# Kernel tuning notes

Measured on AMD Instinct MI355X. Metric: run time of the kernel, lower is better.

Reference implementation:

```python
import jax, jax.numpy as jnp
import numpy as np

DIM = 1024
HEADS = 16
HEAD_DIM = DIM // HEADS
SCALE = DIM ** (-0.5)  # note: module scales by full dim, not head_dim


def setup_inputs() -> dict:
    key = jax.random.key(0)
    k1, k2, k3, k4 = jax.random.split(key, 4)
    B, N = 4, 2048
    x = jax.random.normal(k1, (B, N, DIM), dtype=jnp.float32)
    # nn.Linear(dim, 3*dim, bias=False): weight [3*dim, dim]
    w_qkv = jax.random.normal(k2, (3 * DIM, DIM), dtype=jnp.float32) * (DIM ** -0.5)
    # nn.Linear(dim, dim) with bias
    w_out = jax.random.normal(k3, (DIM, DIM), dtype=jnp.float32) * (DIM ** -0.5)
    b_out = jax.random.normal(k4, (DIM,), dtype=jnp.float32) * 0.01
    return {"x": x, "w_qkv": w_qkv, "w_out": w_out, "b_out": b_out}


def reference(x, w_qkv, w_out, b_out):
    b, n, _ = x.shape
    qkv = jnp.einsum('bnd,ed->bne', x, w_qkv)  # [b, n, 3*dim]
    # rearrange 'b n (qkv h d) -> qkv b h n d'
    qkv = qkv.reshape(b, n, 3, HEADS, HEAD_DIM)
    q, k, v = (qkv[:, :, i].transpose(0, 2, 1, 3) for i in range(3))  # [b, h, n, d]
    dots = jnp.einsum('bhid,bhjd->bhij', q, k) * SCALE
    attn = jax.nn.softmax(dots, axis=-1)
    out = jnp.einsum('bhij,bhjd->bhid', attn, v)
    out = out.transpose(0, 2, 1, 3).reshape(b, n, HEADS * HEAD_DIM)  # [b, n, dim]
    return jnp.einsum('bnd,ed->bne', out, w_out) + b_out
```

## Files before the change

### kernel.cpp

```cpp
#include <hip/hip_runtime.h>

typedef __bf16 bf16_t;
typedef __bf16 bf16x2 __attribute__((ext_vector_type(2)));
typedef __bf16 bf16x4 __attribute__((ext_vector_type(4)));
typedef __bf16 bf16x8 __attribute__((ext_vector_type(8)));
typedef float floatx4 __attribute__((ext_vector_type(4)));

__device__ __forceinline__ void gll16(const void* g, void* l) {
  __builtin_amdgcn_global_load_lds(
      (const __attribute__((address_space(1))) void*)g,
      (__attribute__((address_space(3))) void*)l, 16, 0, 0);
}

__device__ __forceinline__ bf16x8 cvt8(const float4 a, const float4 b) {
  bf16x8 v;
  v[0] = (bf16_t)a.x; v[1] = (bf16_t)a.y; v[2] = (bf16_t)a.z; v[3] = (bf16_t)a.w;
  v[4] = (bf16_t)b.x; v[5] = (bf16_t)b.y; v[6] = (bf16_t)b.z; v[7] = (bf16_t)b.w;
  return v;
}

__global__ __launch_bounds__(256)
void cvt_f32_bf16(const float* __restrict__ src, bf16_t* __restrict__ dst, int n8)
{
  const int i = blockIdx.x * 256 + threadIdx.x;
  if (i < n8) {
    const float4 a = ((const float4*)src)[2 * i];
    const float4 b = ((const float4*)src)[2 * i + 1];
    *(bf16x8*)(dst + (size_t)i * 8) = cvt8(a, b);
  }
}

template<bool A32, bool W32, bool C32>
__global__ __launch_bounds__(256, 2)
void gemm_bt(const void* __restrict__ Av, const void* __restrict__ Wv,
             const float* __restrict__ bias, void* __restrict__ Cv,
             int M, int Nf, int K, int lda)
{
  __shared__ __align__(16) bf16_t lA[128 * 32];
  __shared__ __align__(16) bf16_t lB[128 * 32];

  const int tid  = threadIdx.x;
  const int wave = tid >> 6;
  const int lane = tid & 63;
  const int q    = lane >> 4;
  const int ln   = lane & 15;
  const int wm   = wave >> 1, wn = wave & 1;

  const int mtiles = M >> 7;
  const int mt = blockIdx.x % mtiles;
  const int nt = blockIdx.x / mtiles;
  const int m0 = mt << 7, n0 = nt << 7;

  floatx4 acc[4][4] = {};

  for (int k0 = 0; k0 < K; k0 += 32) {
    if constexpr (A32) {
      const float* Af = (const float*)Av;
#pragma unroll
      for (int sub = 0; sub < 2; ++sub) {
        const int r  = sub * 64 + (tid >> 2);
        const int c8 = tid & 3;
        const float* s = Af + (size_t)(m0 + r) * lda + k0 + c8 * 8;
        const float4 f0 = *(const float4*)s;
        const float4 f1 = *(const float4*)(s + 4);
        *(bf16x8*)(lA + r * 32 + (c8 ^ ((r >> 1) & 3)) * 8) = cvt8(f0, f1);
      }
    } else {
      const bf16_t* Ab = (const bf16_t*)Av;
#pragma unroll
      for (int half = 0; half < 2; ++half) {
        const int rbase = half * 64 + wave * 16;
        const int r  = rbase + (lane >> 2);
        const int gc = (lane & 3) ^ ((r >> 1) & 3);
        gll16(Ab + (size_t)(m0 + r) * lda + k0 + gc * 8, lA + rbase * 32);
      }
    }
    if constexpr (W32) {
      const float* Wf = (const float*)Wv;
#pragma unroll
      for (int sub = 0; sub < 2; ++sub) {
        const int r  = sub * 64 + (tid >> 2);
        const int c8 = tid & 3;
        const float* s = Wf + (size_t)(n0 + r) * K + k0 + c8 * 8;
        const float4 f0 = *(const float4*)s;
        const float4 f1 = *(const float4*)(s + 4);
        *(bf16x8*)(lB + r * 32 + (c8 ^ ((r >> 1) & 3)) * 8) = cvt8(f0, f1);
      }
    } else {
      const bf16_t* Wb = (const bf16_t*)Wv;
#pragma unroll
      for (int half = 0; half < 2; ++half) {
        const int rbase = half * 64 + wave * 16;
        const int r  = rbase + (lane >> 2);
        const int gc = (lane & 3) ^ ((r >> 1) & 3);
        gll16(Wb + (size_t)(n0 + r) * K + k0 + gc * 8, lB + rbase * 32);
      }
    }
    __syncthreads();

    bf16x8 af[4], bfr[4];
#pragma unroll
    for (int i = 0; i < 4; ++i) {
      const int r = wm * 64 + i * 16 + ln;
      af[i] = *(const bf16x8*)(lA + r * 32 + (q ^ ((r >> 1) & 3)) * 8);
    }
#pragma unroll
    for (int j = 0; j < 4; ++j) {
      const int r = wn * 64 + j * 16 + ln;
      bfr[j] = *(const bf16x8*)(lB + r * 32 + (q ^ ((r >> 1) & 3)) * 8);
    }
#pragma unroll
    for (int i = 0; i < 4; ++i)
#pragma unroll
      for (int j = 0; j < 4; ++j)
        acc[i][j] = __builtin_amdgcn_mfma_f32_16x16x32_bf16(af[i], bfr[j], acc[i][j], 0, 0, 0);
    __syncthreads();
  }

#pragma unroll
  for (int j = 0; j < 4; ++j) {
    const int col = n0 + wn * 64 + j * 16 + ln;
    const float bv = bias ? bias[col] : 0.0f;
#pragma unroll
    for (int i = 0; i < 4; ++i) {
      const int row = m0 + wm * 64 + i * 16 + q * 4;
#pragma unroll
      for (int r = 0; r < 4; ++r) {
        const float val = acc[i][j][r] + bv;
        if constexpr (C32)
          ((float*)Cv)[(size_t)(row + r) * Nf + col] = val;
        else
          ((bf16_t*)Cv)[(size_t)(row + r) * Nf + col] = (bf16_t)val;
      }
    }
  }
}

__global__ __launch_bounds__(256, 2)
void attn_kernel(bf16_t* __restrict__ qkv)
{
  __shared__ __align__(16) bf16_t lK[128 * 64];
  __shared__ __align__(16) bf16_t lVT[64 * 128];
  __shared__ __align__(16) bf16_t lP[128 * 136];

  const int tid  = threadIdx.x;
  const int wave = tid >> 6;
  const int lane = tid & 63;
  const int q  = lane >> 4;
  const int ln = lane & 15;
  const int wm = wave >> 1, wn = wave & 1;

  const int bx = blockIdx.x;
  const int qt = bx & 15;
  const int h  = (bx >> 4) & 15;
  const int b  = bx >> 8;

  bf16_t* Qbase = qkv + (size_t)(b * 2048 + qt * 128) * 3072 + h * 64;
  const bf16_t* Kbase = qkv + (size_t)(b * 2048) * 3072 + 1024 + h * 64;
  const bf16_t* Vbase = qkv + (size_t)(b * 2048) * 3072 + 2048 + h * 64;

#pragma unroll
  for (int t = 0; t < 4; ++t) {
    const int rbase = t * 32 + wave * 8;
    const int r  = rbase + (lane >> 3);
    const int gc = (lane & 7) ^ (r & 7);
    gll16(Qbase + (size_t)r * 3072 + gc * 8, lP + rbase * 64);
  }
  __syncthreads();

  bf16x8 qf[4][2];
#pragma unroll
  for (int i = 0; i < 4; ++i) {
    const int r = wm * 64 + i * 16 + ln;
#pragma unroll
    for (int kt = 0; kt < 2; ++kt) {
      const int c = (kt * 4 + q) ^ (r & 7);
      qf[i][kt] = *(const bf16x8*)(lP + r * 64 + c * 8);
    }
  }
  __syncthreads();

  floatx4 accO[4][2] = {};
  floatx4 accS[4] = {};

  bf16x8 ones;
#pragma unroll
  for (int j = 0; j < 8; ++j) ones[j] = (bf16_t)1.0f;

  for (int jt = 0; jt < 16; ++jt) {
    const int j0 = jt * 128;

#pragma unroll
    for (int t = 0; t < 4; ++t) {
      const int rbase = t * 32 + wave * 8;
      const int r  = rbase + (lane >> 3);
      const int gc = (lane & 7) ^ (r & 7);
      gll16(Kbase + (size_t)(j0 + r) * 3072 + gc * 8, lK + rbase * 64);
    }

    {
      const int p = lane;
#pragma unroll
      for (int it = 0; it < 2; ++it) {
        const int c = wave + it * 4;
        const bf16_t* src = Vbase + (size_t)(j0 + 2 * p) * 3072 + c * 8;
        const bf16x8 v0 = *(const bf16x8*)(src);
        const bf16x8 v1 = *(const bf16x8*)(src + 3072);
#pragma unroll
        for (int j = 0; j < 8; ++j) {
          const int d  = c * 8 + j;
          const int ch = (p >> 2) ^ (d & 7);
          bf16x2 pr;
          pr[0] = v0[j];
          pr[1] = v1[j];
          *(bf16x2*)(lVT + d * 128 + ch * 8 + ((2 * p) & 7)) = pr;
        }
      }
    }
    __syncthreads();

    bf16x8 kf[4][2];
#pragma unroll
    for (int n = 0; n < 4; ++n) {
      const int r = wn * 64 + n * 16 + ln;
#pragma unroll
      for (int kt = 0; kt < 2; ++kt) {
        const int c = (kt * 4 + q) ^ (r & 7);
        kf[n][kt] = *(const bf16x8*)(lK + r * 64 + c * 8);
      }
    }
#pragma unroll
    for (int i = 0; i < 4; ++i) {
#pragma unroll
      for (int n = 0; n < 4; ++n) {
        floatx4 st = {0.0f, 0.0f, 0.0f, 0.0f};
        st = __builtin_amdgcn_mfma_f32_16x16x32_bf16(kf[i][0], qf[n][0], st, 0, 0, 0);
        st = __builtin_amdgcn_mfma_f32_16x16x32_bf16(kf[i][1], qf[n][1], st, 0, 0, 0);
        bf16x4 pk;
#pragma unroll
        for (int r = 0; r < 4; ++r)
          pk[r] = (bf16_t)__builtin_amdgcn_exp2f(st[r] * 0.04508422f);
        const int m    = wm * 64 + n * 16 + ln;
        const int tok0 = wn * 64 + i * 16 + q * 4;
        *(bf16x4*)(lP + m * 136 + tok0) = pk;
      }
    }
    __syncthreads();

#pragma unroll
    for (int ks = 0; ks < 4; ++ks) {
      bf16x8 bv[2];
#pragma unroll
      for (int n = 0; n < 2; ++n) {
        const int d  = wn * 32 + n * 16 + ln;
        const int cc = (ks * 4 + q) ^ (d & 7);
        bv[n] = *(const bf16x8*)(lVT + d * 128 + cc * 8);
      }
#pragma unroll
      for (int i = 0; i < 4; ++i) {
        const int m = wm * 64 + i * 16 + ln;
        const bf16x8 ap = *(const bf16x8*)(lP + m * 136 + ks * 32 + q * 8);
        accO[i][0] = __builtin_amdgcn_mfma_f32_16x16x32_bf16(ap, bv[0], accO[i][0], 0, 0, 0);
        accO[i][1] = __builtin_amdgcn_mfma_f32_16x16x32_bf16(ap, bv[1], accO[i][1], 0, 0, 0);
        accS[i]    = __builtin_amdgcn_mfma_f32_16x16x32_bf16(ap, ones,  accS[i],    0, 0, 0);
      }
    }
    __syncthreads();
  }

#pragma unroll
  for (int i = 0; i < 4; ++i) {
#pragma unroll
    for (int r = 0; r < 4; ++r) {
      const int row = wm * 64 + i * 16 + q * 4 + r;
      const float rcp = 1.0f / fmaxf(accS[i][r], 1e-20f);
#pragma unroll
      for (int n = 0; n < 2; ++n) {
        const int col = wn * 32 + n * 16 + ln;
        Qbase[(size_t)row * 3072 + col] = (bf16_t)(accO[i][n][r] * rcp);
      }
    }
  }
}

extern "C" void kernel_launch(void* const* d_in, const int* in_sizes, int n_in,
                              void* d_out, int out_size, void* d_ws, size_t ws_size,
                              hipStream_t stream)
{
  const float* x     = (const float*)d_in[0];
  const float* w_qkv = (const float*)d_in[1];
  const float* w_out = (const float*)d_in[2];
  const float* b_out = (const float*)d_in[3];
  float* out = (float*)d_out;

  bf16_t* qkv    = (bf16_t*)d_ws;
  bf16_t* xb     = qkv    + (size_t)8192 * 3072;
  bf16_t* wqkvb  = xb     + (size_t)8192 * 1024;
  bf16_t* woutb  = wqkvb  + (size_t)3072 * 1024;

  cvt_f32_bf16<<<dim3(4096), dim3(256), 0, stream>>>(x,     xb,    8192 * 1024 / 8);
  cvt_f32_bf16<<<dim3(1536), dim3(256), 0, stream>>>(w_qkv, wqkvb, 3072 * 1024 / 8);
  cvt_f32_bf16<<<dim3(512),  dim3(256), 0, stream>>>(w_out, woutb, 1024 * 1024 / 8);

  gemm_bt<false, false, false><<<dim3(64 * 24), dim3(256), 0, stream>>>(
      xb, wqkvb, nullptr, qkv, 8192, 3072, 1024, 1024);
  attn_kernel<<<dim3(1024), dim3(256), 0, stream>>>(qkv);
  gemm_bt<false, false, true><<<dim3(64 * 8), dim3(256), 0, stream>>>(
      qkv, woutb, b_out, out, 8192, 1024, 1024, 3072);
}
```

Measured before the change: 302.4 us.

## Double-buffer K and register-prefetch V in attention, swizzle P, remap block order

The attention loop now prefetches the next K tile into a second LDS buffer and holds the next V rows in registers, so global loads overlap with the current tile's MFMA work. The trailing barrier per iteration is dropped. The P scratch buffer loses its padding in favour of an XOR swizzle, and s_setprio is raised around MFMA sections. Both GEMM and attention blocks are remapped in a stride-8 interleave to change which tiles run together and improve L2 locality. The cost is more registers and LDS, which may lower occupancy, and a new synchronisation pattern that has to stay correct with one barrier fewer per iteration.

```diff
diff --git a/kernel.cpp b/kernel.cpp
--- a/kernel.cpp
+++ b/kernel.cpp
@@ -46,9 +46,12 @@
   const int ln   = lane & 15;
   const int wm   = wave >> 1, wn = wave & 1;
 
+  const int nwg = gridDim.x;
+  const int bid = (blockIdx.x & 7) * (nwg >> 3) + (blockIdx.x >> 3);
+
   const int mtiles = M >> 7;
-  const int mt = blockIdx.x % mtiles;
-  const int nt = blockIdx.x / mtiles;
+  const int mt = bid % mtiles;
+  const int nt = bid / mtiles;
   const int m0 = mt << 7, n0 = nt << 7;
 
   floatx4 acc[4][4] = {};
@@ -139,9 +142,9 @@
 __global__ __launch_bounds__(256, 2)
 void attn_kernel(bf16_t* __restrict__ qkv)
 {
-  __shared__ __align__(16) bf16_t lK[128 * 64];
+  __shared__ __align__(16) bf16_t lK[2][128 * 64];
   __shared__ __align__(16) bf16_t lVT[64 * 128];
-  __shared__ __align__(16) bf16_t lP[128 * 136];
+  __shared__ __align__(16) bf16_t lP[128 * 128];
 
   const int tid  = threadIdx.x;
   const int wave = tid >> 6;
@@ -150,10 +153,11 @@
   const int ln = lane & 15;
   const int wm = wave >> 1, wn = wave & 1;
 
-  const int bx = blockIdx.x;
-  const int qt = bx & 15;
-  const int h  = (bx >> 4) & 15;
-  const int b  = bx >> 8;
+  const int hw = blockIdx.x;
+  const int w  = (hw & 7) * 128 + (hw >> 3);
+  const int qt = w & 15;
+  const int h  = (w >> 4) & 15;
+  const int b  = w >> 8;
 
   bf16_t* Qbase = qkv + (size_t)(b * 2048 + qt * 128) * 3072 + h * 64;
   const bf16_t* Kbase = qkv + (size_t)(b * 2048) * 3072 + 1024 + h * 64;
@@ -165,6 +169,7 @@
     const int r  = rbase + (lane >> 3);
     const int gc = (lane & 7) ^ (r & 7);
     gll16(Qbase + (size_t)r * 3072 + gc * 8, lP + rbase * 64);
+    gll16(Kbase + (size_t)r * 3072 + gc * 8, lK[0] + rbase * 64);
   }
   __syncthreads();
 
@@ -178,7 +183,14 @@
       qf[i][kt] = *(const bf16x8*)(lP + r * 64 + c * 8);
     }
   }
-  __syncthreads();
+
+  bf16x8 vcur[2][2], vnxt[2][2];
+#pragma unroll
+  for (int it = 0; it < 2; ++it) {
+    const bf16_t* src = Vbase + (size_t)(2 * lane) * 3072 + (wave + it * 4) * 8;
+    vcur[it][0] = *(const bf16x8*)src;
+    vcur[it][1] = *(const bf16x8*)(src + 3072);
+  }
 
   floatx4 accO[4][2] = {};
   floatx4 accS[4] = {};
@@ -188,36 +200,24 @@
   for (int j = 0; j < 8; ++j) ones[j] = (bf16_t)1.0f;
 
   for (int jt = 0; jt < 16; ++jt) {
-    const int j0 = jt * 128;
-
-#pragma unroll
-    for (int t = 0; t < 4; ++t) {
-      const int rbase = t * 32 + wave * 8;
-      const int r  = rbase + (lane >> 3);
-      const int gc = (lane & 7) ^ (r & 7);
-      gll16(Kbase + (size_t)(j0 + r) * 3072 + gc * 8, lK + rbase * 64);
-    }
-
-    {
-      const int p = lane;
-#pragma unroll
-      for (int it = 0; it < 2; ++it) {
-        const int c = wave + it * 4;
-        const bf16_t* src = Vbase + (size_t)(j0 + 2 * p) * 3072 + c * 8;
-        const bf16x8 v0 = *(const bf16x8*)(src);
-        const bf16x8 v1 = *(const bf16x8*)(src + 3072);
-#pragma unroll
-        for (int j = 0; j < 8; ++j) {
-          const int d  = c * 8 + j;
-          const int ch = (p >> 2) ^ (d & 7);
-          bf16x2 pr;
-          pr[0] = v0[j];
-          pr[1] = v1[j];
-          *(bf16x2*)(lVT + d * 128 + ch * 8 + ((2 * p) & 7)) = pr;
-        }
-      }
-    }
+    const bf16_t* lKc = lK[jt & 1];
+    bf16_t*       lKn = lK[(jt & 1) ^ 1];
+
     __syncthreads();
+
+#pragma unroll
+    for (int it = 0; it < 2; ++it) {
+      const int c = wave + it * 4;
+#pragma unroll
+      for (int j = 0; j < 8; ++j) {
+        const int d  = c * 8 + j;
+        const int ch = (lane >> 2) ^ (d & 7);
+        bf16x2 pr;
+        pr[0] = vcur[it][0][j];
+        pr[1] = vcur[it][1][j];
+        *(bf16x2*)(lVT + d * 128 + ch * 8 + ((2 * lane) & 7)) = pr;
+      }
+    }
 
     bf16x8 kf[4][2];
 #pragma unroll
@@ -226,9 +226,28 @@
 #pragma unroll
       for (int kt = 0; kt < 2; ++kt) {
         const int c = (kt * 4 + q) ^ (r & 7);
-        kf[n][kt] = *(const bf16x8*)(lK + r * 64 + c * 8);
-      }
-    }
+        kf[n][kt] = *(const bf16x8*)(lKc + r * 64 + c * 8);
+      }
+    }
+
+    if (jt < 15) {
+      const int j0n = (jt + 1) * 128;
+#pragma unroll
+      for (int t = 0; t < 4; ++t) {
+        const int rbase = t * 32 + wave * 8;
+        const int r  = rbase + (lane >> 3);
+        const int gc = (lane & 7) ^ (r & 7);
+        gll16(Kbase + (size_t)(j0n + r) * 3072 + gc * 8, lKn + rbase * 64);
+      }
+#pragma unroll
+      for (int it = 0; it < 2; ++it) {
+        const bf16_t* src = Vbase + (size_t)(j0n + 2 * lane) * 3072 + (wave + it * 4) * 8;
+        vnxt[it][0] = *(const bf16x8*)src;
+        vnxt[it][1] = *(const bf16x8*)(src + 3072);
+      }
+    }
+
+    __builtin_amdgcn_s_setprio(1);
 #pragma unroll
     for (int i = 0; i < 4; ++i) {
 #pragma unroll
@@ -242,11 +261,14 @@
           pk[r] = (bf16_t)__builtin_amdgcn_exp2f(st[r] * 0.04508422f);
         const int m    = wm * 64 + n * 16 + ln;
         const int tok0 = wn * 64 + i * 16 + q * 4;
-        *(bf16x4*)(lP + m * 136 + tok0) = pk;
-      }
-    }
+        *(bf16x4*)(lP + m * 128 + (((tok0 >> 3) ^ (m & 7)) << 3) + (tok0 & 7)) = pk;
+      }
+    }
+    __builtin_amdgcn_s_setprio(0);
+
     __syncthreads();
 
+    __builtin_amdgcn_s_setprio(1);
 #pragma unroll
     for (int ks = 0; ks < 4; ++ks) {
       bf16x8 bv[2];
@@ -259,13 +281,21 @@
 #pragma unroll
       for (int i = 0; i < 4; ++i) {
         const int m = wm * 64 + i * 16 + ln;
-        const bf16x8 ap = *(const bf16x8*)(lP + m * 136 + ks * 32 + q * 8);
+        const bf16x8 ap = *(const bf16x8*)(lP + m * 128 + (((ks * 4 + q) ^ (m & 7)) << 3));
         accO[i][0] = __builtin_amdgcn_mfma_f32_16x16x32_bf16(ap, bv[0], accO[i][0], 0, 0, 0);
         accO[i][1] = __builtin_amdgcn_mfma_f32_16x16x32_bf16(ap, bv[1], accO[i][1], 0, 0, 0);
         accS[i]    = __builtin_amdgcn_mfma_f32_16x16x32_bf16(ap, ones,  accS[i],    0, 0, 0);
       }
     }
-    __syncthreads();
+    __builtin_amdgcn_s_setprio(0);
+
+    if (jt < 15) {
+#pragma unroll
+      for (int it = 0; it < 2; ++it) {
+        vcur[it][0] = vnxt[it][0];
+        vcur[it][1] = vnxt[it][1];
+      }
+    }
   }
 
 #pragma unroll
```

Result: faster. 292.4 us (-3.3%).
